# Kernel tuning notes

Hardware: AMD Instinct MI355X
Metric: run time of the kernel (lower is better)

Reference implementation:

```python
import math
import jax, jax.numpy as jnp
import numpy as np

EMBED_LEN = 512  # self.dk in the torch module (used for scaling, NOT the head dim)


def setup_inputs() -> dict:
    key = jax.random.key(0)
    kq, kk, kv = jax.random.split(key, 3)
    B, H, S, D = 2, 8, 4096, 64
    queries = jax.random.normal(kq, (B, H, S, D), dtype=jnp.float32)
    keys = jax.random.normal(kk, (B, H, S, D), dtype=jnp.float32)
    # NOTE: values enters as [B, S, H, D]; forward transposes dims (1,2).
    values = jax.random.normal(kv, (B, S, H, D), dtype=jnp.float32)
    return {"queries": queries, "keys": keys, "values": values}


def reference(queries, keys, values):
    # compatibility = Q @ K^T / sqrt(dk), dk = embed_len (512), mask=None branch
    scores = jnp.einsum("bhqd,bhkd->bhqk", queries, keys) / math.sqrt(EMBED_LEN)
    attn = jax.nn.softmax(scores, axis=3)
    # torch.transpose(values, 1, 2): [B,S,H,D] -> [B,H,S,D]
    v = jnp.swapaxes(values, 1, 2)
    return jnp.einsum("bhqk,bhkd->bhqd", attn, v)
```

## Files before the change

kernel.cpp:

```cpp
#include <hip/hip_runtime.h>

typedef __attribute__((ext_vector_type(8))) short bf16x8;
typedef __attribute__((ext_vector_type(4))) short s16x4;
typedef __attribute__((ext_vector_type(4))) float f32x4;

#define MFMA16 __builtin_amdgcn_mfma_f32_16x16x32_bf16

#if __has_builtin(__builtin_amdgcn_exp2f)
__device__ __forceinline__ float exp2_raw(float x) { return __builtin_amdgcn_exp2f(x); }
#else
__device__ __forceinline__ float exp2_raw(float x) {
    float r;
    asm volatile("v_exp_f32 %0, %1" : "=v"(r) : "v"(x));
    return r;
}
#endif

__device__ __forceinline__ short bf16s(float f) {
    __bf16 h = (__bf16)f;
    return __builtin_bit_cast(short, h);
}

__device__ __forceinline__ void gload16(const char* g, char* l) {
    __builtin_amdgcn_global_load_lds(
        (const __attribute__((address_space(1))) unsigned int*)g,
        (__attribute__((address_space(3))) unsigned int*)l, 16, 0, 0);
}

__global__ __launch_bounds__(256) void prep_k(const float* __restrict__ K,
                                              char* __restrict__ Kimg) {
    const int bid = blockIdx.x;
    const int t = threadIdx.x;
    const int c = t & 3, r = t >> 2;
    char* dst = Kimg + (size_t)bid * 8192;
    const float* src = K + (size_t)bid * 4096 + (size_t)r * 64 + c * 16;
    float e[16];
    *(float4*)(e)      = *(const float4*)(src);
    *(float4*)(e + 4)  = *(const float4*)(src + 4);
    *(float4*)(e + 8)  = *(const float4*)(src + 8);
    *(float4*)(e + 12) = *(const float4*)(src + 12);
#pragma unroll
    for (int lg = 0; lg < 4; ++lg) {
        s16x4 wv;
#pragma unroll
        for (int j = 0; j < 4; ++j) wv[j] = bf16s(e[lg * 4 + j]);
        const unsigned f = (unsigned)((((c >> 1) * 4 + lg) ^ (r & 7)));
        *(s16x4*)(dst + r * 128 + f * 16 + (c & 1) * 8) = wv;
    }
}

__global__ __launch_bounds__(256) void prep_v(const float* __restrict__ V,
                                              char* __restrict__ Vimg) {
    const int bid = blockIdx.x;
    const int head = bid >> 6, it = bid & 63;
    const int b = head >> 3, h = head & 7;
    const int t = threadIdx.x;
    const int d = t & 63, f0 = t >> 6;
    char* dst = Vimg + (size_t)bid * 8192;
#pragma unroll
    for (int ff = 0; ff < 2; ++ff) {
        const int f = f0 + ff * 4;
        const int hh = f >> 2, lg = f & 3;
        const int kv0 = hh * 32 + lg * 4;
        const float* src = V + ((size_t)b * 4096 + it * 64 + kv0) * 512 + h * 64 + d;
        bf16x8 wv;
#pragma unroll
        for (int j = 0; j < 4; ++j) wv[j]     = bf16s(src[(size_t)j * 512]);
#pragma unroll
        for (int j = 0; j < 4; ++j) wv[4 + j] = bf16s(src[(size_t)(16 + j) * 512]);
        *(bf16x8*)(dst + d * 128 + (unsigned)((f ^ (d & 7)) * 16)) = wv;
    }
}

__global__ __launch_bounds__(64, 2)
void sdpa_fa_kernel(const float* __restrict__ Q, const char* __restrict__ Kimg,
                    const char* __restrict__ Vimg, float* __restrict__ P0,
                    float* __restrict__ P1, float* __restrict__ LS) {
    __shared__ __align__(16) char LDS[16384];

    const int bid  = blockIdx.x;
    const int xcd  = bid & 7;
    const int idx  = bid >> 3;
    const int head = xcd + 8 * (idx >> 7);
    const int kvh  = (idx >> 6) & 1;
    const int qt   = idx & 63;
    const int hb   = head * 64 + kvh * 32;

    const int l   = threadIdx.x;
    const int lg  = l >> 4;
    const int lc  = l & 15;
    const int lc7 = lc & 7;

    const float C1 = (float)(1.4426950408889634 / 22.627416997969522);

    bf16x8 qf[4][2];
#pragma unroll
    for (int qi = 0; qi < 4; ++qi) {
        const int qrow = qt * 64 + qi * 16 + lc;
        const float* qp = Q + ((size_t)head * 4096 + qrow) * 64;
#pragma unroll
        for (int half = 0; half < 2; ++half) {
            bf16x8 f;
#pragma unroll
            for (int j = 0; j < 4; ++j) {
                f[j]     = bf16s(qp[half * 32 + lg * 4 + j] * C1);
                f[4 + j] = bf16s(qp[half * 32 + 16 + lg * 4 + j] * C1);
            }
            qf[qi][half] = f;
        }
    }

    bf16x8 ones;
#pragma unroll
    for (int j = 0; j < 8; ++j) ones[j] = (short)0x3F80;

    f32x4 Oa[4][4];
    f32x4 ls[4];
#pragma unroll
    for (int qi = 0; qi < 4; ++qi) {
        ls[qi] = (f32x4){0.f, 0.f, 0.f, 0.f};
#pragma unroll
        for (int dt = 0; dt < 4; ++dt) Oa[qi][dt] = (f32x4){0.f, 0.f, 0.f, 0.f};
    }

    unsigned okf[4][2], ovf[4][2];
#pragma unroll
    for (int g = 0; g < 4; ++g) {
        okf[g][0] = (unsigned)((g * 16 + lc) * 128 + (((0 + lg) ^ lc7) * 16));
        okf[g][1] = (unsigned)((g * 16 + lc) * 128 + (((4 + lg) ^ lc7) * 16));
        ovf[g][0] = (unsigned)(8192 + (g * 16 + lc) * 128 + (((0 + lg) ^ lc7) * 16));
        ovf[g][1] = (unsigned)(8192 + (g * 16 + lc) * 128 + (((4 + lg) ^ lc7) * 16));
    }

    auto stage_k = [&](int it) {
        const char* gk = Kimg + (size_t)(hb + it) * 8192 + l * 16;
#pragma unroll
        for (int i = 0; i < 8; ++i) gload16(gk + i * 1024, LDS + i * 1024);
    };
    auto stage_v = [&](int it) {
        const char* gv = Vimg + (size_t)(hb + it) * 8192 + l * 16;
#pragma unroll
        for (int i = 0; i < 8; ++i) gload16(gv + i * 1024, LDS + 8192 + i * 1024);
    };

    stage_k(0);
    stage_v(0);

#pragma unroll 1
    for (int it = 0; it < 32; ++it) {
        const int nx = (it + 1) & 31;

        asm volatile("s_waitcnt vmcnt(8)" ::: "memory");
        __builtin_amdgcn_sched_barrier(0);
        bf16x8 kf[4][2];
#pragma unroll
        for (int g = 0; g < 4; ++g) {
            kf[g][0] = *(const bf16x8*)(LDS + okf[g][0]);
            kf[g][1] = *(const bf16x8*)(LDS + okf[g][1]);
        }
        asm volatile("s_waitcnt lgkmcnt(0)" ::: "memory");
        __builtin_amdgcn_sched_barrier(0);
        stage_k(nx);
        __builtin_amdgcn_sched_barrier(0);

        f32x4 st0[4][2], st1[4][2];
        __builtin_amdgcn_s_setprio(1);
#pragma unroll
        for (int g2 = 0; g2 < 2; ++g2)
#pragma unroll
            for (int qi = 0; qi < 4; ++qi) {
                f32x4 a = (f32x4){0.f, 0.f, 0.f, 0.f};
                a = MFMA16(kf[g2][0], qf[qi][0], a, 0, 0, 0);
                a = MFMA16(kf[g2][1], qf[qi][1], a, 0, 0, 0);
                st0[qi][g2] = a;
            }
#pragma unroll
        for (int g2 = 0; g2 < 2; ++g2)
#pragma unroll
            for (int qi = 0; qi < 4; ++qi) {
                f32x4 a = (f32x4){0.f, 0.f, 0.f, 0.f};
                a = MFMA16(kf[g2 + 2][0], qf[qi][0], a, 0, 0, 0);
                a = MFMA16(kf[g2 + 2][1], qf[qi][1], a, 0, 0, 0);
                st1[qi][g2] = a;
#pragma unroll
                for (int r = 0; r < 4; ++r) st0[qi][g2][r] = exp2_raw(st0[qi][g2][r]);
            }
        __builtin_amdgcn_s_setprio(0);

        bf16x8 pfr0[4];
#pragma unroll
        for (int qi = 0; qi < 4; ++qi) {
            bf16x8 f;
#pragma unroll
            for (int j = 0; j < 4; ++j) {
                f[j]     = bf16s(st0[qi][0][j]);
                f[4 + j] = bf16s(st0[qi][1][j]);
            }
            pfr0[qi] = f;
        }

        asm volatile("s_waitcnt vmcnt(8)" ::: "memory");
        __builtin_amdgcn_sched_barrier(0);
        bf16x8 vf[4][2];
#pragma unroll
        for (int dt = 0; dt < 4; ++dt) {
            vf[dt][0] = *(const bf16x8*)(LDS + ovf[dt][0]);
            vf[dt][1] = *(const bf16x8*)(LDS + ovf[dt][1]);
        }
        asm volatile("s_waitcnt lgkmcnt(0)" ::: "memory");
        __builtin_amdgcn_sched_barrier(0);
        stage_v(nx);
        __builtin_amdgcn_sched_barrier(0);

        __builtin_amdgcn_s_setprio(1);
#pragma unroll
        for (int qi = 0; qi < 4; ++qi) {
            ls[qi] = MFMA16(pfr0[qi], ones, ls[qi], 0, 0, 0);
#pragma unroll
            for (int r = 0; r < 4; ++r) st1[qi][0][r] = exp2_raw(st1[qi][0][r]);
            Oa[qi][0] = MFMA16(pfr0[qi], vf[0][0], Oa[qi][0], 0, 0, 0);
            Oa[qi][1] = MFMA16(pfr0[qi], vf[1][0], Oa[qi][1], 0, 0, 0);
#pragma unroll
            for (int r = 0; r < 4; ++r) st1[qi][1][r] = exp2_raw(st1[qi][1][r]);
            Oa[qi][2] = MFMA16(pfr0[qi], vf[2][0], Oa[qi][2], 0, 0, 0);
            Oa[qi][3] = MFMA16(pfr0[qi], vf[3][0], Oa[qi][3], 0, 0, 0);
        }
        __builtin_amdgcn_s_setprio(0);

        bf16x8 pfr1[4];
#pragma unroll
        for (int qi = 0; qi < 4; ++qi) {
            bf16x8 f;
#pragma unroll
            for (int j = 0; j < 4; ++j) {
                f[j]     = bf16s(st1[qi][0][j]);
                f[4 + j] = bf16s(st1[qi][1][j]);
            }
            pfr1[qi] = f;
        }

        __builtin_amdgcn_s_setprio(1);
#pragma unroll
        for (int qi = 0; qi < 4; ++qi) {
            ls[qi] = MFMA16(pfr1[qi], ones, ls[qi], 0, 0, 0);
#pragma unroll
            for (int dt = 0; dt < 4; ++dt)
                Oa[qi][dt] = MFMA16(pfr1[qi], vf[dt][1], Oa[qi][dt], 0, 0, 0);
        }
        __builtin_amdgcn_s_setprio(0);
    }

    float* P = kvh ? P1 : P0;
    float* lsw = LS + kvh * 65536;
#pragma unroll
    for (int qi = 0; qi < 4; ++qi) {
#pragma unroll
        for (int r = 0; r < 4; ++r) {
            const int q = qt * 64 + qi * 16 + lg * 4 + r;
            float* og = P + ((size_t)head * 4096 + q) * 64 + lc;
#pragma unroll
            for (int dt = 0; dt < 4; ++dt) og[dt * 16] = Oa[qi][dt][r];
            if (lc == 0) lsw[head * 4096 + q] = ls[qi][r];
        }
    }
}

__global__ __launch_bounds__(256) void merge_out(const float* __restrict__ P1,
                                                 const float* __restrict__ LS,
                                                 float* __restrict__ Out) {
    const int i = (blockIdx.x * 256 + threadIdx.x) * 4;
    const int hq = i >> 6;
    const float inv = 1.0f / (LS[hq] + LS[65536 + hq]);
    const float4 a = *(const float4*)(Out + i);
    const float4 b = *(const float4*)(P1 + i);
    float4 r;
    r.x = (a.x + b.x) * inv;
    r.y = (a.y + b.y) * inv;
    r.z = (a.z + b.z) * inv;
    r.w = (a.w + b.w) * inv;
    *(float4*)(Out + i) = r;
}

extern "C" void kernel_launch(void* const* d_in, const int* in_sizes, int n_in,
                              void* d_out, int out_size, void* d_ws, size_t ws_size,
                              hipStream_t stream) {
    const float* Q = (const float*)d_in[0];
    const float* K = (const float*)d_in[1];
    const float* V = (const float*)d_in[2];
    float* Out = (float*)d_out;
    char* Kimg = (char*)d_ws;
    char* Vimg = (char*)d_ws + (size_t)8388608;
    float* P1  = (float*)((char*)d_ws + (size_t)16777216);
    float* LS  = (float*)((char*)d_ws + (size_t)33554432);
    prep_k<<<dim3(1024), dim3(256), 0, stream>>>(K, Kimg);
    prep_v<<<dim3(1024), dim3(256), 0, stream>>>(V, Vimg);
    sdpa_fa_kernel<<<dim3(2048), dim3(64), 0, stream>>>(Q, Kimg, Vimg, Out, P1, LS);
    merge_out<<<dim3(4096), dim3(256), 0, stream>>>(P1, LS, Out);
}
```

Baseline: 93.09 us.

## Split KV into four chunks, store partials in bf16, fuse K/V prep kernels

The attention kernel now divides the KV sequence into four chunks instead of two, so it launches twice as many single-wave blocks, and it halves LDS by sharing one 8KB buffer between K and V tiles in an alternating stage. Partial outputs from chunks 1-3 are written as bf16 to cut write and read traffic, and the merge kernel sums four partials and four row sums. The two prep kernels are fused into one launch. The intent is more parallelism and occupancy. The cost is full vmcnt(0) waits with less prefetch overlap, plus extra rounding error from bf16 partials.

```diff
diff --git a/kernel.cpp b/kernel.cpp
--- a/kernel.cpp
+++ b/kernel.cpp
@@ -27,64 +27,65 @@
         (__attribute__((address_space(3))) unsigned int*)l, 16, 0, 0);
 }
 
-__global__ __launch_bounds__(256) void prep_k(const float* __restrict__ K,
-                                              char* __restrict__ Kimg) {
-    const int bid = blockIdx.x;
+__global__ __launch_bounds__(256) void prep_kv(const float* __restrict__ K,
+                                               const float* __restrict__ V,
+                                               char* __restrict__ Kimg,
+                                               char* __restrict__ Vimg) {
     const int t = threadIdx.x;
-    const int c = t & 3, r = t >> 2;
-    char* dst = Kimg + (size_t)bid * 8192;
-    const float* src = K + (size_t)bid * 4096 + (size_t)r * 64 + c * 16;
-    float e[16];
-    *(float4*)(e)      = *(const float4*)(src);
-    *(float4*)(e + 4)  = *(const float4*)(src + 4);
-    *(float4*)(e + 8)  = *(const float4*)(src + 8);
-    *(float4*)(e + 12) = *(const float4*)(src + 12);
-#pragma unroll
-    for (int lg = 0; lg < 4; ++lg) {
-        s16x4 wv;
-#pragma unroll
-        for (int j = 0; j < 4; ++j) wv[j] = bf16s(e[lg * 4 + j]);
-        const unsigned f = (unsigned)((((c >> 1) * 4 + lg) ^ (r & 7)));
-        *(s16x4*)(dst + r * 128 + f * 16 + (c & 1) * 8) = wv;
-    }
-}
-
-__global__ __launch_bounds__(256) void prep_v(const float* __restrict__ V,
-                                              char* __restrict__ Vimg) {
-    const int bid = blockIdx.x;
-    const int head = bid >> 6, it = bid & 63;
-    const int b = head >> 3, h = head & 7;
-    const int t = threadIdx.x;
-    const int d = t & 63, f0 = t >> 6;
-    char* dst = Vimg + (size_t)bid * 8192;
-#pragma unroll
-    for (int ff = 0; ff < 2; ++ff) {
-        const int f = f0 + ff * 4;
-        const int hh = f >> 2, lg = f & 3;
-        const int kv0 = hh * 32 + lg * 4;
-        const float* src = V + ((size_t)b * 4096 + it * 64 + kv0) * 512 + h * 64 + d;
-        bf16x8 wv;
-#pragma unroll
-        for (int j = 0; j < 4; ++j) wv[j]     = bf16s(src[(size_t)j * 512]);
-#pragma unroll
-        for (int j = 0; j < 4; ++j) wv[4 + j] = bf16s(src[(size_t)(16 + j) * 512]);
-        *(bf16x8*)(dst + d * 128 + (unsigned)((f ^ (d & 7)) * 16)) = wv;
+    if (blockIdx.x < 1024) {
+        const int bid = blockIdx.x;
+        const int c = t & 3, r = t >> 2;
+        char* dst = Kimg + (size_t)bid * 8192;
+        const float* src = K + (size_t)bid * 4096 + (size_t)r * 64 + c * 16;
+        float e[16];
+        *(float4*)(e)      = *(const float4*)(src);
+        *(float4*)(e + 4)  = *(const float4*)(src + 4);
+        *(float4*)(e + 8)  = *(const float4*)(src + 8);
+        *(float4*)(e + 12) = *(const float4*)(src + 12);
+#pragma unroll
+        for (int lg = 0; lg < 4; ++lg) {
+            s16x4 wv;
+#pragma unroll
+            for (int j = 0; j < 4; ++j) wv[j] = bf16s(e[lg * 4 + j]);
+            const unsigned f = (unsigned)((((c >> 1) * 4 + lg) ^ (r & 7)));
+            *(s16x4*)(dst + r * 128 + f * 16 + (c & 1) * 8) = wv;
+        }
+    } else {
+        const int bid = blockIdx.x - 1024;
+        const int head = bid >> 6, it = bid & 63;
+        const int b = head >> 3, h = head & 7;
+        const int d = t & 63, f0 = t >> 6;
+        char* dst = Vimg + (size_t)bid * 8192;
+#pragma unroll
+        for (int ff = 0; ff < 2; ++ff) {
+            const int f = f0 + ff * 4;
+            const int hh = f >> 2, lg = f & 3;
+            const int kv0 = hh * 32 + lg * 4;
+            const float* src = V + ((size_t)b * 4096 + it * 64 + kv0) * 512 + h * 64 + d;
+            bf16x8 wv;
+#pragma unroll
+            for (int j = 0; j < 4; ++j) wv[j]     = bf16s(src[(size_t)j * 512]);
+#pragma unroll
+            for (int j = 0; j < 4; ++j) wv[4 + j] = bf16s(src[(size_t)(16 + j) * 512]);
+            *(bf16x8*)(dst + d * 128 + (unsigned)((f ^ (d & 7)) * 16)) = wv;
+        }
     }
 }
 
 __global__ __launch_bounds__(64, 2)
 void sdpa_fa_kernel(const float* __restrict__ Q, const char* __restrict__ Kimg,
                     const char* __restrict__ Vimg, float* __restrict__ P0,
-                    float* __restrict__ P1, float* __restrict__ LS) {
-    __shared__ __align__(16) char LDS[16384];
+                    unsigned short* __restrict__ Pb, float* __restrict__ LS) {
+    __shared__ __align__(16) char LDS[8192];
 
     const int bid  = blockIdx.x;
     const int xcd  = bid & 7;
     const int idx  = bid >> 3;
-    const int head = xcd + 8 * (idx >> 7);
-    const int kvh  = (idx >> 6) & 1;
-    const int qt   = idx & 63;
-    const int hb   = head * 64 + kvh * 32;
+    const int head = xcd + 8 * (idx >> 8);
+    const int rem  = idx & 255;
+    const int kvh  = rem >> 6;
+    const int qt   = rem & 63;
+    const int hb   = head * 64 + kvh * 16;
 
     const int l   = threadIdx.x;
     const int lg  = l >> 4;
@@ -123,13 +124,11 @@
         for (int dt = 0; dt < 4; ++dt) Oa[qi][dt] = (f32x4){0.f, 0.f, 0.f, 0.f};
     }
 
-    unsigned okf[4][2], ovf[4][2];
+    unsigned off0[4], off1[4];
 #pragma unroll
     for (int g = 0; g < 4; ++g) {
-        okf[g][0] = (unsigned)((g * 16 + lc) * 128 + (((0 + lg) ^ lc7) * 16));
-        okf[g][1] = (unsigned)((g * 16 + lc) * 128 + (((4 + lg) ^ lc7) * 16));
-        ovf[g][0] = (unsigned)(8192 + (g * 16 + lc) * 128 + (((0 + lg) ^ lc7) * 16));
-        ovf[g][1] = (unsigned)(8192 + (g * 16 + lc) * 128 + (((4 + lg) ^ lc7) * 16));
+        off0[g] = (unsigned)((g * 16 + lc) * 128 + (((0 + lg) ^ lc7) * 16));
+        off1[g] = (unsigned)((g * 16 + lc) * 128 + (((4 + lg) ^ lc7) * 16));
     }
 
     auto stage_k = [&](int it) {
@@ -140,27 +139,26 @@
     auto stage_v = [&](int it) {
         const char* gv = Vimg + (size_t)(hb + it) * 8192 + l * 16;
 #pragma unroll
-        for (int i = 0; i < 8; ++i) gload16(gv + i * 1024, LDS + 8192 + i * 1024);
+        for (int i = 0; i < 8; ++i) gload16(gv + i * 1024, LDS + i * 1024);
     };
 
     stage_k(0);
-    stage_v(0);
 
 #pragma unroll 1
-    for (int it = 0; it < 32; ++it) {
-        const int nx = (it + 1) & 31;
-
-        asm volatile("s_waitcnt vmcnt(8)" ::: "memory");
+    for (int it = 0; it < 16; ++it) {
+        const int nx = (it + 1) & 15;
+
+        asm volatile("s_waitcnt vmcnt(0)" ::: "memory");
         __builtin_amdgcn_sched_barrier(0);
         bf16x8 kf[4][2];
 #pragma unroll
         for (int g = 0; g < 4; ++g) {
-            kf[g][0] = *(const bf16x8*)(LDS + okf[g][0]);
-            kf[g][1] = *(const bf16x8*)(LDS + okf[g][1]);
+            kf[g][0] = *(const bf16x8*)(LDS + off0[g]);
+            kf[g][1] = *(const bf16x8*)(LDS + off1[g]);
         }
         asm volatile("s_waitcnt lgkmcnt(0)" ::: "memory");
         __builtin_amdgcn_sched_barrier(0);
-        stage_k(nx);
+        stage_v(it);
         __builtin_amdgcn_sched_barrier(0);
 
         f32x4 st0[4][2], st1[4][2];
@@ -199,17 +197,17 @@
             pfr0[qi] = f;
         }
 
-        asm volatile("s_waitcnt vmcnt(8)" ::: "memory");
+        asm volatile("s_waitcnt vmcnt(0)" ::: "memory");
         __builtin_amdgcn_sched_barrier(0);
         bf16x8 vf[4][2];
 #pragma unroll
         for (int dt = 0; dt < 4; ++dt) {
-            vf[dt][0] = *(const bf16x8*)(LDS + ovf[dt][0]);
-            vf[dt][1] = *(const bf16x8*)(LDS + ovf[dt][1]);
+            vf[dt][0] = *(const bf16x8*)(LDS + off0[dt]);
+            vf[dt][1] = *(const bf16x8*)(LDS + off1[dt]);
         }
         asm volatile("s_waitcnt lgkmcnt(0)" ::: "memory");
         __builtin_amdgcn_sched_barrier(0);
-        stage_v(nx);
+        stage_k(nx);
         __builtin_amdgcn_sched_barrier(0);
 
         __builtin_amdgcn_s_setprio(1);
@@ -250,34 +248,52 @@
         __builtin_amdgcn_s_setprio(0);
     }
 
-    float* P = kvh ? P1 : P0;
     float* lsw = LS + kvh * 65536;
-#pragma unroll
-    for (int qi = 0; qi < 4; ++qi) {
-#pragma unroll
-        for (int r = 0; r < 4; ++r) {
-            const int q = qt * 64 + qi * 16 + lg * 4 + r;
-            float* og = P + ((size_t)head * 4096 + q) * 64 + lc;
-#pragma unroll
-            for (int dt = 0; dt < 4; ++dt) og[dt * 16] = Oa[qi][dt][r];
-            if (lc == 0) lsw[head * 4096 + q] = ls[qi][r];
-        }
-    }
-}
-
-__global__ __launch_bounds__(256) void merge_out(const float* __restrict__ P1,
+    if (kvh == 0) {
+#pragma unroll
+        for (int qi = 0; qi < 4; ++qi)
+#pragma unroll
+            for (int r = 0; r < 4; ++r) {
+                const int q = qt * 64 + qi * 16 + lg * 4 + r;
+                float* og = P0 + ((size_t)head * 4096 + q) * 64 + lc;
+#pragma unroll
+                for (int dt = 0; dt < 4; ++dt) og[dt * 16] = Oa[qi][dt][r];
+                if (lc == 0) lsw[head * 4096 + q] = ls[qi][r];
+            }
+    } else {
+        unsigned short* Pq = Pb + (size_t)(kvh - 1) * 4194304;
+#pragma unroll
+        for (int qi = 0; qi < 4; ++qi)
+#pragma unroll
+            for (int r = 0; r < 4; ++r) {
+                const int q = qt * 64 + qi * 16 + lg * 4 + r;
+                unsigned short* og = Pq + ((size_t)head * 4096 + q) * 64 + lc;
+#pragma unroll
+                for (int dt = 0; dt < 4; ++dt)
+                    og[dt * 16] = (unsigned short)bf16s(Oa[qi][dt][r]);
+                if (lc == 0) lsw[head * 4096 + q] = ls[qi][r];
+            }
+    }
+}
+
+__global__ __launch_bounds__(256) void merge_out(const unsigned short* __restrict__ Pb,
                                                  const float* __restrict__ LS,
                                                  float* __restrict__ Out) {
     const int i = (blockIdx.x * 256 + threadIdx.x) * 4;
     const int hq = i >> 6;
-    const float inv = 1.0f / (LS[hq] + LS[65536 + hq]);
+    const float inv = 1.0f / (LS[hq] + LS[65536 + hq] + LS[131072 + hq] + LS[196608 + hq]);
     const float4 a = *(const float4*)(Out + i);
-    const float4 b = *(const float4*)(P1 + i);
+    float s[4] = {a.x, a.y, a.z, a.w};
+#pragma unroll
+    for (int p = 0; p < 3; ++p) {
+        ushort4 u = *(const ushort4*)(Pb + (size_t)p * 4194304 + i);
+        s[0] += __builtin_bit_cast(float, (unsigned)u.x << 16);
+        s[1] += __builtin_bit_cast(float, (unsigned)u.y << 16);
+        s[2] += __builtin_bit_cast(float, (unsigned)u.z << 16);
+        s[3] += __builtin_bit_cast(float, (unsigned)u.w << 16);
+    }
     float4 r;
-    r.x = (a.x + b.x) * inv;
-    r.y = (a.y + b.y) * inv;
-    r.z = (a.z + b.z) * inv;
-    r.w = (a.w + b.w) * inv;
+    r.x = s[0] * inv; r.y = s[1] * inv; r.z = s[2] * inv; r.w = s[3] * inv;
     *(float4*)(Out + i) = r;
 }
 
@@ -290,10 +306,9 @@
     float* Out = (float*)d_out;
     char* Kimg = (char*)d_ws;
     char* Vimg = (char*)d_ws + (size_t)8388608;
-    float* P1  = (float*)((char*)d_ws + (size_t)16777216);
-    float* LS  = (float*)((char*)d_ws + (size_t)33554432);
-    prep_k<<<dim3(1024), dim3(256), 0, stream>>>(K, Kimg);
-    prep_v<<<dim3(1024), dim3(256), 0, stream>>>(V, Vimg);
-    sdpa_fa_kernel<<<dim3(2048), dim3(64), 0, stream>>>(Q, Kimg, Vimg, Out, P1, LS);
-    merge_out<<<dim3(4096), dim3(256), 0, stream>>>(P1, LS, Out);
-}
+    unsigned short* Pb = (unsigned short*)((char*)d_ws + 16777216);
+    float* LS = (float*)((char*)d_ws + (size_t)41943040);
+    prep_kv<<<dim3(2048), dim3(256), 0, stream>>>(K, V, Kimg, Vimg);
+    sdpa_fa_kernel<<<dim3(4096), dim3(64), 0, stream>>>(Q, Kimg, Vimg, Out, Pb, LS);
+    merge_out<<<dim3(4096), dim3(256), 0, stream>>>(Pb, LS, Out);
+}
```

After: 95.58 us. 2.7% more time.
